# Optimization experiments

Hardware: AMD Instinct MI355X
Metric: run time of the kernel (lower is better)

Reference implementation:

```python
import jax, jax.numpy as jnp
import numpy as np

N_EXPERTS = 16
DS_DIM = 3

def _conv2d(x, w):
    # x: [B,C,H,W], w: [O,I,kH,kW], VALID, stride 1
    return jax.lax.conv_general_dilated(x, w, (1, 1), 'VALID',
                                        dimension_numbers=('NCHW', 'OIHW', 'NCHW'))

def _maxpool2(x):
    return jax.lax.reduce_window(x, -jnp.inf, jax.lax.max,
                                 (1, 1, 2, 2), (1, 1, 2, 2), 'VALID')

def _forward(x, conv1_w, conv1_b, conv2_w, conv2_b,
             fc1_w, fc1_b, fc2_w, fc2_b, fc3_w, fc3_b,
             fc4_w, fc4_b, fc5_w, fc5_b, B_mats, C_mats, x_tar):
    bsz = x.shape[0]
    img = x[:, DS_DIM:].reshape(bsz, 1, 64, 64)
    h = _maxpool2(jax.nn.relu(_conv2d(img, conv1_w) + conv1_b[None, :, None, None]))
    h = _maxpool2(jax.nn.relu(_conv2d(h, conv2_w) + conv2_b[None, :, None, None]))
    h = h.reshape(bsz, -1)                      # [B, 1690]
    h = jnp.concatenate([h, x[:, :DS_DIM]], axis=1)  # [B, 1693]
    h = jax.nn.relu(h @ fc1_w.T + fc1_b)
    h = jax.nn.relu(h @ fc2_w.T + fc2_b)
    h = jax.nn.relu(h @ fc3_w.T + fc3_b)
    h = jax.nn.relu(h @ fc4_w.T + fc4_b)
    w_all = jax.nn.softmax(h @ fc5_w.T + fc5_b, axis=1)   # [B, N]
    A = B_mats + C_mats                          # [N, d, d]
    diff = x_tar - x[:, :DS_DIM]                 # [B, d]
    # torch: sum_i w[:,i,None] * (A_i @ diff.T).T == einsum over experts
    s_all = jnp.einsum('bn,nij,bj->bi', w_all, A, diff)
    return s_all


def setup_inputs() -> dict:
    key = jax.random.key(0)
    ks = jax.random.split(key, 20)
    rn = lambda k, shp, s: jax.random.normal(k, shp, dtype=jnp.float32) * s
    d = {}
    d['x'] = rn(ks[0], (8192, 4099), 1.0)
    d['conv1_w'] = rn(ks[1], (5, 1, 5, 5), 0.2)
    d['conv1_b'] = rn(ks[2], (5,), 0.05)
    d['conv2_w'] = rn(ks[3], (10, 5, 5, 5), 0.09)
    d['conv2_b'] = rn(ks[4], (10,), 0.05)
    d['fc1_w'] = rn(ks[5], (512, 1693), 1.0 / np.sqrt(1693))
    d['fc1_b'] = rn(ks[6], (512,), 0.02)
    d['fc2_w'] = rn(ks[7], (256, 512), 1.0 / np.sqrt(512))
    d['fc2_b'] = rn(ks[8], (256,), 0.02)
    d['fc3_w'] = rn(ks[9], (128, 256), 1.0 / np.sqrt(256))
    d['fc3_b'] = rn(ks[10], (128,), 0.02)
    d['fc4_w'] = rn(ks[11], (64, 128), 1.0 / np.sqrt(128))
    d['fc4_b'] = rn(ks[12], (64,), 0.02)
    d['fc5_w'] = rn(ks[13], (N_EXPERTS, 64), 1.0 / np.sqrt(64))
    d['fc5_b'] = rn(ks[14], (N_EXPERTS,), 0.02)
    # geotorch constrains B to PSD and C to skew-symmetric; build such mats
    G = rn(ks[15], (N_EXPERTS, DS_DIM, DS_DIM), 0.5)
    d['B_mats'] = jnp.einsum('nij,nkj->nik', G, G)        # PSD
    S = rn(ks[16], (N_EXPERTS, DS_DIM, DS_DIM), 0.5)
    d['C_mats'] = S - jnp.swapaxes(S, 1, 2)               # skew
    d['x_tar'] = jnp.zeros((1, DS_DIM), dtype=jnp.float32)
    return d


def reference(x, conv1_w, conv1_b, conv2_w, conv2_b,
              fc1_w, fc1_b, fc2_w, fc2_b, fc3_w, fc3_b,
              fc4_w, fc4_b, fc5_w, fc5_b, B_mats, C_mats, x_tar):
    return _forward(x, conv1_w, conv1_b, conv2_w, conv2_b,
                    fc1_w, fc1_b, fc2_w, fc2_b, fc3_w, fc3_b,
                    fc4_w, fc4_b, fc5_w, fc5_b, B_mats, C_mats, x_tar)
```

## Files before the change

### kernel.cpp

```cpp
#include <hip/hip_runtime.h>
#include <hip/hip_bf16.h>
#include <hip/hip_fp16.h>
#include <math.h>

#define XW 4099
#define DSD 3
#define BSZ 8192
#define KP1 1696

typedef __attribute__((ext_vector_type(8))) _Float16 f16x8;
typedef __attribute__((ext_vector_type(4))) float    f32x4;

static __device__ __forceinline__ short f2h(float f) {
    union { _Float16 h; short s; } u;
    u.h = (_Float16)f;
    return u.s;
}

#define C0 (512 * KP1)
#define C1 (C0 + 256 * 512)
#define C2 (C1 + 128 * 256)
#define C3 (C2 + 64 * 128)
__global__ __launch_bounds__(256) void cvt_all(
    const float* __restrict__ w1s, short* __restrict__ w1d,
    const float* __restrict__ w2s, short* __restrict__ w2d,
    const float* __restrict__ w3s, short* __restrict__ w3d,
    const float* __restrict__ w4s, short* __restrict__ w4d)
{
    const int i = blockIdx.x * 256 + threadIdx.x;
    if (i < C0) {
        const int n = i / KP1, k = i % KP1;
        w1d[i] = (k < 1693) ? f2h(w1s[(size_t)n * 1693 + k]) : (short)0;
    } else if (i < C1) {
        const int j = i - C0; w2d[j] = f2h(w2s[j]);
    } else if (i < C2) {
        const int j = i - C1; w3d[j] = f2h(w3s[j]);
    } else if (i < C3) {
        const int j = i - C2; w4d[j] = f2h(w4s[j]);
    }
}

__global__ __launch_bounds__(256, 4) void conv_fused(
    const float* __restrict__ x,
    const float* __restrict__ w1, const float* __restrict__ b1,
    const float* __restrict__ w2, const float* __restrict__ b2,
    short* __restrict__ act1)
{
    __shared__ __align__(16) char smem0[64 * 68 * 4];
    float     (*img)[68]  = (float(*)[68])smem0;
    _Float16  (*w2f)[232] = (_Float16(*)[232])smem0;

    __shared__ __align__(16) _Float16  h1[30][30][8];
    __shared__ __align__(16) float     cw1[5][28];
    __shared__ float cb1[5];
    __shared__ float cb2s[16];
    __shared__ __align__(16) int kofft[28];

    const int b = blockIdx.x;
    const int t = threadIdx.x;

    const float* xr = x + (size_t)b * XW + DSD;
    #pragma unroll
    for (int i = 0; i < 16; ++i) {
        const int idx = t + 256 * i;
        img[idx >> 6][idx & 63] = xr[idx];
    }
    {
        uint4* h1z = (uint4*)&h1[0][0][0];
        const uint4 z4 = {0u, 0u, 0u, 0u};
        #pragma unroll
        for (int i = 0; i < 4; ++i) {
            const int idx = t + 256 * i;
            if (idx < 900) h1z[idx] = z4;
        }
    }
    if (t < 140) { const int c = t / 28, k = t % 28; cw1[c][k] = (k < 25) ? w1[c * 25 + k] : 0.f; }
    if (t >= 144 && t < 149) cb1[t - 144] = b1[t - 144];
    if (t >= 160 && t < 176) cb2s[t - 160] = (t - 160 < 10) ? b2[t - 160] : 0.f;
    if (t >= 192 && t < 220) {
        const int p = t - 192;
        kofft[p] = (p < 25) ? (p / 5) * 480 + (p % 5) * 16 : 0;
    }
    __syncthreads();

    if (t < 225) {
        const int ty = t / 15, tx = t % 15;
        const int y0 = 4 * ty, x0 = 4 * tx;
        f32x4 pv[8][2];
        #pragma unroll
        for (int r = 0; r < 8; ++r) {
            pv[r][0] = *(const f32x4*)&img[y0 + r][x0];
            pv[r][1] = *(const f32x4*)&img[y0 + r][x0 + 4];
        }
        asm volatile("" :
            "+v"(pv[0][0]), "+v"(pv[0][1]), "+v"(pv[1][0]), "+v"(pv[1][1]),
            "+v"(pv[2][0]), "+v"(pv[2][1]), "+v"(pv[3][0]), "+v"(pv[3][1]),
            "+v"(pv[4][0]), "+v"(pv[4][1]), "+v"(pv[5][0]), "+v"(pv[5][1]),
            "+v"(pv[6][0]), "+v"(pv[6][1]), "+v"(pv[7][0]), "+v"(pv[7][1]));
        #pragma unroll 1
        for (int c = 0; c < 5; ++c) {
            f32x4 wv4[7];
            #pragma unroll
            for (int i = 0; i < 7; ++i) wv4[i] = *(const f32x4*)&cw1[c][4 * i];
            const float bias = cb1[c];
            float acc[4][4];
            #pragma unroll
            for (int cy = 0; cy < 4; ++cy)
                #pragma unroll
                for (int cx = 0; cx < 4; ++cx) acc[cy][cx] = bias;
            #pragma unroll
            for (int ky = 0; ky < 5; ++ky)
                #pragma unroll
                for (int kx = 0; kx < 5; ++kx) {
                    const int kk = ky * 5 + kx;
                    const float wv = wv4[kk >> 2][kk & 3];
                    #pragma unroll
                    for (int cy = 0; cy < 4; ++cy)
                        #pragma unroll
                        for (int cx = 0; cx < 4; ++cx) {
                            const int px = cx + kx;
                            acc[cy][cx] += pv[cy + ky][px >> 2][px & 3] * wv;
                        }
                }
            #pragma unroll
            for (int sy = 0; sy < 2; ++sy)
                #pragma unroll
                for (int sx = 0; sx < 2; ++sx) {
                    const float m = fmaxf(
                        fmaxf(acc[2 * sy][2 * sx],     acc[2 * sy][2 * sx + 1]),
                        fmaxf(acc[2 * sy + 1][2 * sx], acc[2 * sy + 1][2 * sx + 1]));
                    h1[2 * ty + sy][2 * tx + sx][c] = (_Float16)fmaxf(m, 0.f);
                }
        }
    }
    __syncthreads();

    for (int i = t; i < 448; i += 256) {
        const int wc = i / 28, wp = i % 28;
        f16x8 cell;
        #pragma unroll
        for (int ic = 0; ic < 8; ++ic) cell[ic] = (_Float16)0.f;
        if (wc < 10 && wp < 25) {
            #pragma unroll
            for (int ic = 0; ic < 5; ++ic)
                cell[ic] = (_Float16)w2[(wc * 5 + ic) * 25 + wp];
        }
        *(f16x8*)&w2f[wc][wp * 8] = cell;
    }
    __syncthreads();

    short* outr = act1 + (size_t)b * KP1;
    {
        const int wv_ = t >> 6, lane = t & 63;
        const int lr = lane & 15, kg = lane >> 4;
        const float bias2 = cb2s[lr];
        const int qa = lr & 3;
        const int wa_off = lr >> 2;

        int bases[11];
        #pragma unroll
        for (int u = 0; u < 11; ++u) {
            const int tt = u * 4 + wv_;
            int w_A = tt * 4 + wa_off;
            w_A = (w_A < 169) ? w_A : 168;
            const int Y = (w_A * 5042) >> 16;
            const int X = w_A - Y * 13;
            bases[u] = (2 * Y + (qa & 1)) * 480 + (2 * X + (qa >> 1)) * 16;
        }

        f32x4 acc[11];
        #pragma unroll
        for (int u = 0; u < 11; ++u) acc[u] = (f32x4){0.f, 0.f, 0.f, 0.f};

        const char* h1p = (const char*)&h1[0][0][0];

        #pragma unroll 1
        for (int s = 0; s < 7; ++s) {
            const int koffp = kofft[s * 4 + kg];
            const f16x8 bfs = *(const f16x8*)&w2f[lr][s * 32 + kg * 8];
            #pragma unroll
            for (int u = 0; u < 11; ++u) {
                const f16x8 af = *(const f16x8*)(h1p + (bases[u] + koffp));
                acc[u] = __builtin_amdgcn_mfma_f32_16x16x32_f16(af, bfs, acc[u], 0, 0, 0);
            }
        }

        #pragma unroll
        for (int u = 0; u < 11; ++u) {
            const int tt = u * 4 + wv_;
            const int w_C = tt * 4 + kg;
            if (lr < 10 && w_C < 169) {
                const float m = fmaxf(fmaxf(acc[u][0], acc[u][1]), fmaxf(acc[u][2], acc[u][3]));
                outr[lr * 169 + w_C] = f2h(fmaxf(m + bias2, 0.f));
            }
        }
    }
    if (t < DSD)           outr[1690 + t] = f2h(x[(size_t)b * XW + t]);
    if (t >= DSD && t < 6) outr[1690 + t] = 0;
}

template <int RELU, int OUTH>
__global__ __launch_bounds__(256) void mfma_fc(
    const short* __restrict__ A,
    const short* __restrict__ W,
    const float* __restrict__ bias,
    void* __restrict__ Cout,
    int N, int Kp)
{
    __shared__ __align__(16) short As[64][40];
    __shared__ __align__(16) short Ws[64][40];

    const int tid  = threadIdx.x;
    const int m0   = blockIdx.y * 64;
    const int n0   = blockIdx.x * 64;
    const int wv   = tid >> 6, lane = tid & 63;
    const int rm   = (wv >> 1) * 32, rn = (wv & 1) * 32;
    const int lr   = lane & 15, kg = lane >> 4;
    const int sr   = tid >> 2, sc = (tid & 3) * 8;

    f32x4 acc[2][2];
    #pragma unroll
    for (int i = 0; i < 2; ++i)
        #pragma unroll
        for (int j = 0; j < 2; ++j)
            #pragma unroll
            for (int q = 0; q < 4; ++q) acc[i][j][q] = 0.f;

    for (int k0 = 0; k0 < Kp; k0 += 32) {
        *(uint4*)&As[sr][sc] = *(const uint4*)&A[(size_t)(m0 + sr) * Kp + k0 + sc];
        *(uint4*)&Ws[sr][sc] = *(const uint4*)&W[(size_t)(n0 + sr) * Kp + k0 + sc];
        __syncthreads();
        f16x8 aF[2], bF[2];
        #pragma unroll
        for (int mi = 0; mi < 2; ++mi) aF[mi] = *(const f16x8*)&As[rm + mi * 16 + lr][kg * 8];
        #pragma unroll
        for (int nj = 0; nj < 2; ++nj) bF[nj] = *(const f16x8*)&Ws[rn + nj * 16 + lr][kg * 8];
        #pragma unroll
        for (int mi = 0; mi < 2; ++mi)
            #pragma unroll
            for (int nj = 0; nj < 2; ++nj)
                acc[mi][nj] = __builtin_amdgcn_mfma_f32_16x16x32_f16(
                    aF[mi], bF[nj], acc[mi][nj], 0, 0, 0);
        __syncthreads();
    }

    #pragma unroll
    for (int mi = 0; mi < 2; ++mi)
        #pragma unroll
        for (int nj = 0; nj < 2; ++nj) {
            const int col  = n0 + rn + nj * 16 + lr;
            const int rowb = m0 + rm + mi * 16 + kg * 4;
            const float bv = bias[col];
            #pragma unroll
            for (int q = 0; q < 4; ++q) {
                float v = acc[mi][nj][q] + bv;
                if (RELU) v = fmaxf(v, 0.f);
                if (OUTH) ((short*)Cout)[(size_t)(rowb + q) * N + col] = f2h(v);
                else      ((float*)Cout)[(size_t)(rowb + q) * N + col] = v;
            }
        }
}

__global__ __launch_bounds__(256) void head_kernel(
    const float* __restrict__ act5, const float* __restrict__ w5,
    const float* __restrict__ b5, const float* __restrict__ Bm,
    const float* __restrict__ Cm, const float* __restrict__ x,
    const float* __restrict__ x_tar, float* __restrict__ out)
{
    __shared__ float sw[16 * 64];
    __shared__ float sb[16];
    __shared__ float sA[16 * 9];
    __shared__ float st[3];
    const int t = threadIdx.x;
    for (int i = t; i < 1024; i += 256) sw[i] = w5[i];
    if (t < 16)  sb[t] = b5[t];
    if (t < 144) sA[t] = Bm[t] + Cm[t];
    if (t < 3)   st[t] = x_tar[t];
    __syncthreads();

    const int b = blockIdx.x * 256 + t;
    float h[64];
    const float* ar = act5 + (size_t)b * 64;
    #pragma unroll
    for (int i = 0; i < 64; ++i) h[i] = ar[i];

    float logit[16];
    float mx = -1e30f;
    #pragma unroll
    for (int n = 0; n < 16; ++n) {
        float s = sb[n];
        const float* wr = sw + n * 64;
        #pragma unroll
        for (int i = 0; i < 64; ++i) s += h[i] * wr[i];
        logit[n] = s;
        mx = fmaxf(mx, s);
    }
    float sum = 0.f;
    #pragma unroll
    for (int n = 0; n < 16; ++n) { logit[n] = __expf(logit[n] - mx); sum += logit[n]; }
    const float inv = 1.f / sum;

    const float d0 = st[0] - x[(size_t)b * XW + 0];
    const float d1 = st[1] - x[(size_t)b * XW + 1];
    const float d2 = st[2] - x[(size_t)b * XW + 2];
    float s0 = 0.f, s1 = 0.f, s2 = 0.f;
    #pragma unroll
    for (int n = 0; n < 16; ++n) {
        const float w = logit[n] * inv;
        const float* An = sA + n * 9;
        s0 += w * (An[0] * d0 + An[1] * d1 + An[2] * d2);
        s1 += w * (An[3] * d0 + An[4] * d1 + An[5] * d2);
        s2 += w * (An[6] * d0 + An[7] * d1 + An[8] * d2);
    }
    out[(size_t)b * 3 + 0] = s0;
    out[(size_t)b * 3 + 1] = s1;
    out[(size_t)b * 3 + 2] = s2;
}

extern "C" void kernel_launch(void* const* d_in, const int* in_sizes, int n_in,
                              void* d_out, int out_size, void* d_ws, size_t ws_size,
                              hipStream_t stream) {
    const float* x       = (const float*)d_in[0];
    const float* conv1_w = (const float*)d_in[1];
    const float* conv1_b = (const float*)d_in[2];
    const float* conv2_w = (const float*)d_in[3];
    const float* conv2_b = (const float*)d_in[4];
    const float* fc1_w   = (const float*)d_in[5];
    const float* fc1_b   = (const float*)d_in[6];
    const float* fc2_w   = (const float*)d_in[7];
    const float* fc2_b   = (const float*)d_in[8];
    const float* fc3_w   = (const float*)d_in[9];
    const float* fc3_b   = (const float*)d_in[10];
    const float* fc4_w   = (const float*)d_in[11];
    const float* fc4_b   = (const float*)d_in[12];
    const float* fc5_w   = (const float*)d_in[13];
    const float* fc5_b   = (const float*)d_in[14];
    const float* B_mats  = (const float*)d_in[15];
    const float* C_mats  = (const float*)d_in[16];
    const float* x_tar   = (const float*)d_in[17];
    float* out = (float*)d_out;

    char* p = (char*)d_ws;
    short* act1 = (short*)p;  p += (size_t)BSZ * KP1 * 2;
    short* act2 = (short*)p;  p += (size_t)BSZ * 512 * 2;
    short* act3 = (short*)p;  p += (size_t)BSZ * 256 * 2;
    short* act4 = (short*)p;  p += (size_t)BSZ * 128 * 2;
    float* act5 = (float*)p;  p += (size_t)BSZ * 64 * 4;
    short* w1h  = (short*)p;  p += (size_t)512 * KP1 * 2;
    short* w2h  = (short*)p;  p += (size_t)256 * 512 * 2;
    short* w3h  = (short*)p;  p += (size_t)128 * 256 * 2;
    short* w4h  = (short*)p;  p += (size_t)64 * 128 * 2;

    cvt_all<<<(C3 + 255) / 256, 256, 0, stream>>>(
        fc1_w, w1h, fc2_w, w2h, fc3_w, w3h, fc4_w, w4h);

    conv_fused<<<BSZ, 256, 0, stream>>>(x, conv1_w, conv1_b, conv2_w, conv2_b, act1);

    mfma_fc<1, 1><<<dim3(512 / 64, BSZ / 64), 256, 0, stream>>>(act1, w1h, fc1_b, act2, 512, KP1);
    mfma_fc<1, 1><<<dim3(256 / 64, BSZ / 64), 256, 0, stream>>>(act2, w2h, fc2_b, act3, 256, 512);
    mfma_fc<1, 1><<<dim3(128 / 64, BSZ / 64), 256, 0, stream>>>(act3, w3h, fc3_b, act4, 128, 256);
    mfma_fc<1, 0><<<dim3(64 / 64,  BSZ / 64), 256, 0, stream>>>(act4, w4h, fc4_b, act5, 64, 128);

    head_kernel<<<BSZ / 256, 256, 0, stream>>>(act5, fc5_w, fc5_b, B_mats, C_mats, x, x_tar, out);
}
```

Baseline: 211.3 us.

## Compute conv1 with fp16 MFMA im2col instead of scalar FMA tiles

Replaces the per-thread fp32 scalar 5x5 convolution for conv1 with an MFMA 16x16x32 fp16 formulation. The image is stored in shared memory as fp16, plus a second copy shifted by one column so odd-column patches stay 4-byte aligned. The 5x5 filters are packed into a padded 8x8 layout split across two MFMA k-chunks, and each MFMA output row group is max-pooled directly. This cuts the FMA instruction count of conv1 in exchange for an fp16 input rounding and extra shared-memory traffic and zero-fill.

```diff
diff --git a/kernel.cpp b/kernel.cpp
--- a/kernel.cpp
+++ b/kernel.cpp
@@ -46,36 +46,49 @@
     const float* __restrict__ w2, const float* __restrict__ b2,
     short* __restrict__ act1)
 {
-    __shared__ __align__(16) char smem0[64 * 68 * 4];
-    float     (*img)[68]  = (float(*)[68])smem0;
-    _Float16  (*w2f)[232] = (_Float16(*)[232])smem0;
-
-    __shared__ __align__(16) _Float16  h1[30][30][8];
-    __shared__ __align__(16) float     cw1[5][28];
-    __shared__ float cb1[5];
+    __shared__ __align__(16) char smem0[2 * 68 * 68 * 2];
+    _Float16 (*imgA)[68] = (_Float16(*)[68])smem0;
+    _Float16 (*imgB)[68] = (_Float16(*)[68])(smem0 + 9248);
+    _Float16 (*w2f)[232] = (_Float16(*)[232])smem0;
+
+    __shared__ __align__(16) _Float16 h1[30][30][8];
+    __shared__ __align__(16) _Float16 w1f[16][72];
+    __shared__ float cb1s[16];
     __shared__ float cb2s[16];
     __shared__ __align__(16) int kofft[28];
 
     const int b = blockIdx.x;
     const int t = threadIdx.x;
 
-    const float* xr = x + (size_t)b * XW + DSD;
-    #pragma unroll
-    for (int i = 0; i < 16; ++i) {
-        const int idx = t + 256 * i;
-        img[idx >> 6][idx & 63] = xr[idx];
-    }
     {
+        uint4* z = (uint4*)smem0;
+        const uint4 z4 = {0u, 0u, 0u, 0u};
+        #pragma unroll
+        for (int i = 0; i < 5; ++i) {
+            const int idx = t + 256 * i;
+            if (idx < 1156) z[idx] = z4;
+        }
         uint4* h1z = (uint4*)&h1[0][0][0];
-        const uint4 z4 = {0u, 0u, 0u, 0u};
         #pragma unroll
         for (int i = 0; i < 4; ++i) {
             const int idx = t + 256 * i;
             if (idx < 900) h1z[idx] = z4;
         }
     }
-    if (t < 140) { const int c = t / 28, k = t % 28; cw1[c][k] = (k < 25) ? w1[c * 25 + k] : 0.f; }
-    if (t >= 144 && t < 149) cb1[t - 144] = b1[t - 144];
+    if (t < 128) {
+        const int ch = t >> 3, k0 = (t & 7) * 8;
+        f16x8 cell;
+        #pragma unroll
+        for (int j = 0; j < 8; ++j) {
+            const int k = k0 + j;
+            const int ky = (k >> 5) * 4 + ((k >> 3) & 3);
+            const int kx = k & 7;
+            cell[j] = (ch < 5 && ky < 5 && kx < 5)
+                    ? (_Float16)w1[ch * 25 + ky * 5 + kx] : (_Float16)0.f;
+        }
+        *(f16x8*)&w1f[ch][k0] = cell;
+    }
+    if (t >= 128 && t < 144) cb1s[t - 128] = (t - 128 < 5) ? b1[t - 128] : 0.f;
     if (t >= 160 && t < 176) cb2s[t - 160] = (t - 160 < 10) ? b2[t - 160] : 0.f;
     if (t >= 192 && t < 220) {
         const int p = t - 192;
@@ -83,54 +96,50 @@
     }
     __syncthreads();
 
-    if (t < 225) {
-        const int ty = t / 15, tx = t % 15;
-        const int y0 = 4 * ty, x0 = 4 * tx;
-        f32x4 pv[8][2];
-        #pragma unroll
-        for (int r = 0; r < 8; ++r) {
-            pv[r][0] = *(const f32x4*)&img[y0 + r][x0];
-            pv[r][1] = *(const f32x4*)&img[y0 + r][x0 + 4];
-        }
-        asm volatile("" :
-            "+v"(pv[0][0]), "+v"(pv[0][1]), "+v"(pv[1][0]), "+v"(pv[1][1]),
-            "+v"(pv[2][0]), "+v"(pv[2][1]), "+v"(pv[3][0]), "+v"(pv[3][1]),
-            "+v"(pv[4][0]), "+v"(pv[4][1]), "+v"(pv[5][0]), "+v"(pv[5][1]),
-            "+v"(pv[6][0]), "+v"(pv[6][1]), "+v"(pv[7][0]), "+v"(pv[7][1]));
+    const float* xr = x + (size_t)b * XW + DSD;
+    #pragma unroll
+    for (int i = 0; i < 16; ++i) {
+        const int idx = t + 256 * i;
+        const int yy = idx >> 6, xx = idx & 63;
+        const _Float16 v = (_Float16)xr[idx];
+        imgA[yy][xx] = v;
+        if (xx > 0) imgB[yy][xx - 1] = v;
+    }
+    __syncthreads();
+
+    {
+        const int lane = t & 63, wv_ = t >> 6;
+        const int lr = lane & 15, kg = lane >> 4;
+        const int wa = lr >> 2;
+        const int dy = lr & 1, dx = (lr >> 1) & 1;
+        const f16x8 bf0 = *(const f16x8*)&w1f[lr][kg * 8];
+        const f16x8 bf1 = *(const f16x8*)&w1f[lr][32 + kg * 8];
+        const char* base0 = dx ? (const char*)&imgB[0][0] : (const char*)&imgA[0][0];
+        const float bias1 = cb1s[lr];
+        const int r0 = kg * 136;
+        const int r1 = (4 + kg) * 136;
+
         #pragma unroll 1
-        for (int c = 0; c < 5; ++c) {
-            f32x4 wv4[7];
-            #pragma unroll
-            for (int i = 0; i < 7; ++i) wv4[i] = *(const f32x4*)&cw1[c][4 * i];
-            const float bias = cb1[c];
-            float acc[4][4];
-            #pragma unroll
-            for (int cy = 0; cy < 4; ++cy)
-                #pragma unroll
-                for (int cx = 0; cx < 4; ++cx) acc[cy][cx] = bias;
-            #pragma unroll
-            for (int ky = 0; ky < 5; ++ky)
-                #pragma unroll
-                for (int kx = 0; kx < 5; ++kx) {
-                    const int kk = ky * 5 + kx;
-                    const float wv = wv4[kk >> 2][kk & 3];
-                    #pragma unroll
-                    for (int cy = 0; cy < 4; ++cy)
-                        #pragma unroll
-                        for (int cx = 0; cx < 4; ++cx) {
-                            const int px = cx + kx;
-                            acc[cy][cx] += pv[cy + ky][px >> 2][px & 3] * wv;
-                        }
-                }
-            #pragma unroll
-            for (int sy = 0; sy < 2; ++sy)
-                #pragma unroll
-                for (int sx = 0; sx < 2; ++sx) {
-                    const float m = fmaxf(
-                        fmaxf(acc[2 * sy][2 * sx],     acc[2 * sy][2 * sx + 1]),
-                        fmaxf(acc[2 * sy + 1][2 * sx], acc[2 * sy + 1][2 * sx + 1]));
-                    h1[2 * ty + sy][2 * tx + sx][c] = (_Float16)fmaxf(m, 0.f);
-                }
+        for (int tt = wv_; tt < 225; tt += 4) {
+            const int w_A = tt * 4 + wa;
+            const int wyA = (w_A * 2185) >> 16;
+            const int wxA = w_A - wyA * 30;
+            const char* pb = base0 + (2 * wyA + dy) * 136 + wxA * 4;
+            union { f16x8 v; unsigned u[4]; } A0, A1;
+            #pragma unroll
+            for (int j = 0; j < 4; ++j) A0.u[j] = *(const unsigned*)(pb + r0 + 4 * j);
+            #pragma unroll
+            for (int j = 0; j < 4; ++j) A1.u[j] = *(const unsigned*)(pb + r1 + 4 * j);
+            f32x4 acc = {0.f, 0.f, 0.f, 0.f};
+            acc = __builtin_amdgcn_mfma_f32_16x16x32_f16(A0.v, bf0, acc, 0, 0, 0);
+            acc = __builtin_amdgcn_mfma_f32_16x16x32_f16(A1.v, bf1, acc, 0, 0, 0);
+            if (lr < 5) {
+                const int w_C = tt * 4 + kg;
+                const int wyC = (w_C * 2185) >> 16;
+                const int wxC = w_C - wyC * 30;
+                const float m = fmaxf(fmaxf(acc[0], acc[1]), fmaxf(acc[2], acc[3]));
+                h1[wyC][wxC][lr] = (_Float16)fmaxf(m + bias1, 0.f);
+            }
         }
     }
     __syncthreads();
@@ -201,10 +210,8 @@
 
 template <int RELU, int OUTH>
 __global__ __launch_bounds__(256) void mfma_fc(
-    const short* __restrict__ A,
-    const short* __restrict__ W,
-    const float* __restrict__ bias,
-    void* __restrict__ Cout,
+    const short* __restrict__ A, const short* __restrict__ W,
+    const float* __restrict__ bias, void* __restrict__ Cout,
     int N, int Kp)
 {
     __shared__ __align__(16) short As[64][40];
```

New measurement: 279.7 us. 32.4% more time.
